# Performance work log

Hardware: AMD Instinct MI355X
Metric: run time of the kernel (lower is better)

The kernel has to match this reference:

```python
import jax, jax.numpy as jnp
import numpy as np

N_NODES, N_EDGES = 50000, 800000
D_H, D_E, HID = 128, 64, 128  # dim_in = D_H + D_E = 192; hidden_dim2 = D_H + HID = 256


def setup_inputs() -> dict:
    key = jax.random.key(0)
    k1, k2, k3, k4, k5 = jax.random.split(key, 5)
    H = jax.random.normal(k1, (N_NODES, D_H), dtype=jnp.float32)
    idx = jax.random.randint(k2, (2, N_EDGES), 0, N_NODES)
    X_e = jax.random.normal(k3, (N_EDGES, D_E), dtype=jnp.float32)
    # kaiming_normal (fan_in mode, relu gain): std = sqrt(2 / fan_in)
    W1 = jax.random.normal(k4, (D_H + D_E, HID), dtype=jnp.float32) * np.sqrt(2.0 / (D_H + D_E)).astype(np.float32)
    W2 = jax.random.normal(k5, (D_H + HID, HID), dtype=jnp.float32) * np.sqrt(2.0 / (D_H + HID)).astype(np.float32)
    return {"H": H, "idx": idx, "X_e": X_e, "W1": W1, "W2": W2}


def reference(H, idx, X_e, W1, W2):
    # gather source-node embeddings and concat with edge features: [E, d_h + d_e]
    x = jnp.concatenate([H[idx[0]], X_e], axis=1)
    y = jax.nn.relu(x @ W1)                                   # [E, HID]
    # scatter_max into destination nodes; empty segments -> 0 (torch_scatter zero fill).
    y = jax.ops.segment_max(y, idx[1], num_segments=H.shape[0])
    y = jnp.maximum(y, 0.0)  # relu output >= 0, so this only fixes -inf empties
    y = jnp.concatenate([H, y], axis=1)                       # [N, d_h + HID]
    y = jax.nn.relu(y @ W2)                                   # [N, HID]
    return y + H  # residual connection (HID == d_h)
```

## Files before the change

kernel.cpp:

```cpp
#include <hip/hip_runtime.h>
#include <hip/hip_bf16.h>
#include <stdint.h>

#define N_NODES 50000
#define N_EDGES 800000
#define D_H 128
#define D_E 64
#define HID 128

#define MTILE 96
#define SMAX 16
#define N_ETILES ((N_EDGES + MTILE - 1) / MTILE)

#define SCAN_B 512
#define N_CHUNKS ((N_NODES + SCAN_B - 1) / SCAN_B)

typedef __attribute__((ext_vector_type(8))) short bf16x8;
typedef __attribute__((ext_vector_type(4))) short s16x4;
typedef __attribute__((ext_vector_type(4))) float f32x4;
typedef __attribute__((ext_vector_type(4))) int i32x4;

__device__ __forceinline__ unsigned short f2bf(float x) {
    unsigned int u = __float_as_uint(x);
    u += 0x7FFFu + ((u >> 16) & 1u);
    return (unsigned short)(u >> 16);
}

__device__ __forceinline__ bf16x8 pack8(const f32x4 a, const f32x4 b) {
    bf16x8 o = { (short)f2bf(a[0]), (short)f2bf(a[1]), (short)f2bf(a[2]), (short)f2bf(a[3]),
                 (short)f2bf(b[0]), (short)f2bf(b[1]), (short)f2bf(b[2]), (short)f2bf(b[3]) };
    return o;
}

#define NG4 (N_NODES * HID / 4)
#define ND4 (N_NODES / 4)
__global__ void zero_ws(float* __restrict__ gmax, int* __restrict__ deg) {
    const int i = blockIdx.x * blockDim.x + threadIdx.x;
    if (i < NG4) {
        ((f32x4*)gmax)[i] = f32x4{0.f, 0.f, 0.f, 0.f};
    } else if (i < NG4 + ND4) {
        ((i32x4*)deg)[i - NG4] = i32x4{0, 0, 0, 0};
    }
}

#define NHB4 (N_NODES * D_H / 4)
#define NW1 (192 * HID)
#define NW2 (256 * HID)
__global__ void conv_aux(const float* __restrict__ H,
                         const float* __restrict__ W1,
                         const float* __restrict__ W2,
                         unsigned short* __restrict__ Hb,
                         unsigned short* __restrict__ W1t,
                         unsigned short* __restrict__ W2t) {
    const int i = blockIdx.x * blockDim.x + threadIdx.x;
    if (i < NHB4) {
        const f32x4 v = ((const f32x4*)H)[i];
        s16x4 pkv = { (short)f2bf(v[0]), (short)f2bf(v[1]),
                      (short)f2bf(v[2]), (short)f2bf(v[3]) };
        ((s16x4*)Hb)[i] = pkv;
    } else if (i < NHB4 + NW1) {
        const int j = i - NHB4;
        const int n = j / 192, k = j - n * 192;
        W1t[j] = f2bf(W1[k * HID + n]);
    } else if (i < NHB4 + NW1 + NW2) {
        const int j = i - NHB4 - NW1;
        const int n = j >> 8, k = j & 255;
        W2t[j] = f2bf(W2[k * HID + n]);
    }
}

__global__ void hist(const int* __restrict__ idx, int* __restrict__ deg) {
    const int i = blockIdx.x * blockDim.x + threadIdx.x;
    atomicAdd(&deg[idx[N_EDGES + i]], 1);
}

__global__ void scan_a(const int* __restrict__ deg, int* __restrict__ sc,
                       int* __restrict__ totals) {
    __shared__ int s[SCAN_B];
    const int tid = threadIdx.x;
    const int i = blockIdx.x * SCAN_B + tid;
    const int v = (i < N_NODES) ? deg[i] : 0;
    s[tid] = v;
    __syncthreads();
    for (int o = 1; o < SCAN_B; o <<= 1) {
        int t = (tid >= o) ? s[tid - o] : 0;
        __syncthreads();
        s[tid] += t;
        __syncthreads();
    }
    if (i < N_NODES) sc[i] = s[tid] - v;
    if (tid == SCAN_B - 1) totals[blockIdx.x] = s[SCAN_B - 1];
}

__global__ void scan_b(int* __restrict__ totals) {
    __shared__ int s[128];
    const int tid = threadIdx.x;
    const int v = (tid < N_CHUNKS) ? totals[tid] : 0;
    s[tid] = v;
    __syncthreads();
    for (int o = 1; o < 128; o <<= 1) {
        int t = (tid >= o) ? s[tid - o] : 0;
        __syncthreads();
        s[tid] += t;
        __syncthreads();
    }
    if (tid < N_CHUNKS) totals[tid] = s[tid] - v;
}

__global__ void scan_c(const int* __restrict__ sc, const int* __restrict__ totals,
                       int* __restrict__ cursor) {
    const int i = blockIdx.x * SCAN_B + threadIdx.x;
    if (i < N_NODES) cursor[i] = sc[i] + totals[blockIdx.x];
}

__global__ void scatter(const int* __restrict__ idx, int* __restrict__ cursor,
                        unsigned long long* __restrict__ pk8) {
    int i = blockIdx.x * blockDim.x + threadIdx.x;
    const int s = idx[i];
    const int d = idx[N_EDGES + i];
    const int p = atomicAdd(&cursor[d], 1);
    pk8[p] = (unsigned long long)(unsigned)i |
             ((unsigned long long)(unsigned)s << 20) |
             ((unsigned long long)(unsigned)d << 37);
}

__global__ __launch_bounds__(256, 3)
void edge_sorted(const float* __restrict__ H,
                 const unsigned short* __restrict__ Hb,
                 const float* __restrict__ Xe,
                 const float* __restrict__ W1,
                 const unsigned short* __restrict__ W1t,
                 const unsigned long long* __restrict__ pk8,
                 float* __restrict__ gmax, int useAux) {
    __shared__ unsigned short sX[MTILE][200];
    __shared__ float ymax[SMAX + 1][132];
    __shared__ int rowD[MTILE];
    __shared__ int segNode[SMAX];
    __shared__ int sWaveTot[4];
    __shared__ unsigned char rowG[MTILE];

    const int tid  = threadIdx.x;
    const int wave = tid >> 6;
    const int lane = tid & 63;
    const int p0   = blockIdx.x * MTILE;

    const int col = lane & 15;
    const int kr0 = (lane >> 4) * 8;

    if (useAux) {
        #pragma unroll
        for (int it = 0; it < 6; ++it) {
            const int j   = tid + it * 256;
            const int row = j >> 4;
            const int c8  = (j & 15) * 8;
            int pe = p0 + row; if (pe >= N_EDGES) pe = N_EDGES - 1;
            const int src = (int)((pk8[pe] >> 20) & 0x1FFFFull);
            *(bf16x8*)&sX[row][c8] = *(const bf16x8*)(Hb + (size_t)src * D_H + c8);
        }
    } else {
        #pragma unroll
        for (int it = 0; it < 12; ++it) {
            const int j   = tid + it * 256;
            const int row = j >> 5;
            const int c4  = (j & 31) * 4;
            int pe = p0 + row; if (pe >= N_EDGES) pe = N_EDGES - 1;
            const int src = (int)((pk8[pe] >> 20) & 0x1FFFFull);
            const f32x4 v = *(const f32x4*)(H + (size_t)src * D_H + c4);
            s16x4 pkv = { (short)f2bf(v[0]), (short)f2bf(v[1]),
                          (short)f2bf(v[2]), (short)f2bf(v[3]) };
            *(s16x4*)&sX[row][c4] = pkv;
        }
    }
    #pragma unroll
    for (int it = 0; it < 3; ++it) {
        const int j   = tid + it * 256;
        const int row = j >> 3;
        const int c8  = (j & 7) * 8;
        int pe = p0 + row; if (pe >= N_EDGES) pe = N_EDGES - 1;
        const int e = (int)(pk8[pe] & 0xFFFFFull);
        const float* p = Xe + (size_t)e * D_E + c8;
        *(bf16x8*)&sX[row][128 + c8] = pack8(*(const f32x4*)p, *(const f32x4*)(p + 4));
    }

    bf16x8 bfrag[6][2];
    if (useAux) {
        #pragma unroll
        for (int ks = 0; ks < 6; ++ks)
            #pragma unroll
            for (int nf = 0; nf < 2; ++nf) {
                const int n = wave * 32 + nf * 16 + col;
                bfrag[ks][nf] = *(const bf16x8*)&W1t[(size_t)n * 192 + ks * 32 + kr0];
            }
    } else {
        #pragma unroll
        for (int ks = 0; ks < 6; ++ks)
            #pragma unroll
            for (int nf = 0; nf < 2; ++nf) {
                const int n  = wave * 32 + nf * 16 + col;
                const int kb = ks * 32 + kr0;
                bf16x8 b;
                #pragma unroll
                for (int f = 0; f < 8; ++f) b[f] = (short)f2bf(W1[(kb + f) * HID + n]);
                bfrag[ks][nf] = b;
            }
    }

    const int pe0 = p0 + tid;
    const bool inTile = (tid < MTILE);
    const bool valid  = inTile && (pe0 < N_EDGES);
    int d = 0;
    if (inTile) {
        const int pc = valid ? pe0 : (N_EDGES - 1);
        d = (int)(pk8[pc] >> 37);
        rowD[tid] = d;
    }
    int dp = __shfl_up(d, 1);
    if (lane == 0 && inTile && tid > 0) dp = (int)(pk8[pe0 - 1] >> 37);
    const bool flag = valid && (tid == 0 || d != dp);
    const unsigned long long m = __ballot(flag);
    if (lane == 0) sWaveTot[wave] = (int)__popcll(m);

    for (int i2 = tid; i2 < (SMAX + 1) * 132; i2 += 256) ((float*)ymax)[i2] = 0.f;
    __syncthreads();

    int g = 255;
    if (valid) {
        const unsigned long long le =
            (lane == 63) ? ~0ull : ((1ull << (lane + 1)) - 1);
        g = (int)__popcll(m & le) - 1 + ((wave == 1) ? sWaveTot[0] : 0);
    }
    if (inTile) rowG[tid] = (unsigned char)(valid ? g : 255);
    if (flag && g < SMAX) segNode[g] = d;
    __syncthreads();

    f32x4 acc[6][2];
    #pragma unroll
    for (int mm = 0; mm < 6; ++mm) {
        acc[mm][0] = f32x4{0.f, 0.f, 0.f, 0.f};
        acc[mm][1] = f32x4{0.f, 0.f, 0.f, 0.f};
    }
    const int arow = lane & 15;
    __builtin_amdgcn_s_setprio(1);
    #pragma unroll
    for (int ks = 0; ks < 6; ++ks)
        #pragma unroll
        for (int mm = 0; mm < 6; ++mm) {
            bf16x8 a = *(const bf16x8*)&sX[mm * 16 + arow][ks * 32 + kr0];
            acc[mm][0] = __builtin_amdgcn_mfma_f32_16x16x32_bf16(a, bfrag[ks][0], acc[mm][0], 0, 0, 0);
            acc[mm][1] = __builtin_amdgcn_mfma_f32_16x16x32_bf16(a, bfrag[ks][1], acc[mm][1], 0, 0, 0);
        }
    __builtin_amdgcn_s_setprio(0);

    const int rb = (lane >> 4) * 4;
    const int cb = wave * 32 + col;
    #pragma unroll
    for (int mm = 0; mm < 6; ++mm) {
        const int r0 = mm * 16 + rb;
        const int g0 = rowG[r0];
        const int g3 = rowG[r0 + 3];
        if (g0 == g3) {
            const float v0 = fmaxf(fmaxf(acc[mm][0][0], acc[mm][0][1]),
                                   fmaxf(acc[mm][0][2], acc[mm][0][3]));
            const float v1 = fmaxf(fmaxf(acc[mm][1][0], acc[mm][1][1]),
                                   fmaxf(acc[mm][1][2], acc[mm][1][3]));
            if (g0 < SMAX) {
                if (v0 > 0.f) atomicMax((int*)&ymax[g0][cb],      __float_as_int(v0));
                if (v1 > 0.f) atomicMax((int*)&ymax[g0][cb + 16], __float_as_int(v1));
            } else if (g0 < 255) {
                float* base = gmax + (size_t)rowD[r0] * HID;
                if (v0 > 0.f) atomicMax((int*)(base + cb),      __float_as_int(v0));
                if (v1 > 0.f) atomicMax((int*)(base + cb + 16), __float_as_int(v1));
            }
        } else {
            #pragma unroll
            for (int r = 0; r < 4; ++r) {
                const int gg = rowG[r0 + r];
                const float v0 = acc[mm][0][r];
                const float v1 = acc[mm][1][r];
                if (gg < SMAX) {
                    if (v0 > 0.f) atomicMax((int*)&ymax[gg][cb],      __float_as_int(v0));
                    if (v1 > 0.f) atomicMax((int*)&ymax[gg][cb + 16], __float_as_int(v1));
                } else if (gg < 255) {
                    float* base = gmax + (size_t)rowD[r0 + r] * HID;
                    if (v0 > 0.f) atomicMax((int*)(base + cb),      __float_as_int(v0));
                    if (v1 > 0.f) atomicMax((int*)(base + cb + 16), __float_as_int(v1));
                }
            }
        }
    }
    __syncthreads();

    const int nSeg = sWaveTot[0] + sWaveTot[1];
    const int nS = (nSeg < SMAX) ? nSeg : SMAX;
    for (int i2 = tid; i2 < nS * 128; i2 += 256) {
        const int sg = i2 >> 7;
        const int c  = i2 & 127;
        const float v = ymax[sg][c];
        float* dst = gmax + (size_t)segNode[sg] * HID + c;
        if (sg == 0 || sg == nSeg - 1) {
            if (v > 0.f) atomicMax((int*)dst, __float_as_int(v));
        } else {
            *dst = v;
        }
    }
}

__global__ __launch_bounds__(256, 4)
void node_mlp(const float* __restrict__ H,
              const float* __restrict__ gmax,
              const float* __restrict__ W2,
              const unsigned short* __restrict__ W2t,
              float* __restrict__ out, int useAux) {
    __shared__ unsigned short sA[64][264];

    const int tid  = threadIdx.x;
    const int wave = tid >> 6;
    const int lane = tid & 63;
    const int base = blockIdx.x * 64;

    const int col = lane & 15;
    const int kr0 = (lane >> 4) * 8;
    bf16x8 bfrag[8][2];
    if (useAux) {
        #pragma unroll
        for (int ks = 0; ks < 8; ++ks)
            #pragma unroll
            for (int nf = 0; nf < 2; ++nf) {
                const int n = wave * 32 + nf * 16 + col;
                bfrag[ks][nf] = *(const bf16x8*)&W2t[(size_t)n * 256 + ks * 32 + kr0];
            }
    } else {
        #pragma unroll
        for (int ks = 0; ks < 8; ++ks)
            #pragma unroll
            for (int nf = 0; nf < 2; ++nf) {
                const int n  = wave * 32 + nf * 16 + col;
                const int kb = ks * 32 + kr0;
                bf16x8 b;
                #pragma unroll
                for (int f = 0; f < 8; ++f) b[f] = (short)f2bf(W2[(kb + f) * HID + n]);
                bfrag[ks][nf] = b;
            }
    }

    #pragma unroll
    for (int it = 0; it < 8; ++it) {
        const int i   = tid + it * 256;
        const int row = i >> 5;
        const int c4  = (i & 31) * 4;
        int node = base + row;
        if (node >= N_NODES) node = N_NODES - 1;
        const f32x4 v = *(const f32x4*)(H + (size_t)node * D_H + c4);
        s16x4 pkv = { (short)f2bf(v[0]), (short)f2bf(v[1]),
                      (short)f2bf(v[2]), (short)f2bf(v[3]) };
        *(s16x4*)&sA[row][c4] = pkv;
    }
    #pragma unroll
    for (int it = 0; it < 8; ++it) {
        const int i   = tid + it * 256;
        const int row = i >> 5;
        const int c4  = (i & 31) * 4;
        int node = base + row;
        if (node >= N_NODES) node = N_NODES - 1;
        const f32x4 v = *(const f32x4*)(gmax + (size_t)node * HID + c4);
        s16x4 pkv = { (short)f2bf(v[0]), (short)f2bf(v[1]),
                      (short)f2bf(v[2]), (short)f2bf(v[3]) };
        *(s16x4*)&sA[row][128 + c4] = pkv;
    }
    __syncthreads();

    f32x4 acc[4][2];
    #pragma unroll
    for (int mm = 0; mm < 4; ++mm) {
        acc[mm][0] = f32x4{0.f, 0.f, 0.f, 0.f};
        acc[mm][1] = f32x4{0.f, 0.f, 0.f, 0.f};
    }
    const int arow = lane & 15;
    __builtin_amdgcn_s_setprio(1);
    #pragma unroll
    for (int ks = 0; ks < 8; ++ks)
        #pragma unroll
        for (int mm = 0; mm < 4; ++mm) {
            bf16x8 a = *(const bf16x8*)&sA[mm * 16 + arow][ks * 32 + kr0];
            acc[mm][0] = __builtin_amdgcn_mfma_f32_16x16x32_bf16(a, bfrag[ks][0], acc[mm][0], 0, 0, 0);
            acc[mm][1] = __builtin_amdgcn_mfma_f32_16x16x32_bf16(a, bfrag[ks][1], acc[mm][1], 0, 0, 0);
        }
    __builtin_amdgcn_s_setprio(0);

    const int rb = (lane >> 4) * 4;
    #pragma unroll
    for (int mm = 0; mm < 4; ++mm)
        #pragma unroll
        for (int r = 0; r < 4; ++r) {
            const int node = base + mm * 16 + rb + r;
            if (node < N_NODES) {
                const size_t o = (size_t)node * HID + wave * 32 + col;
                out[o]      = fmaxf(acc[mm][0][r], 0.f) + H[o];
                out[o + 16] = fmaxf(acc[mm][1][r], 0.f) + H[o + 16];
            }
        }
}

extern "C" void kernel_launch(void* const* d_in, const int* in_sizes, int n_in,
                              void* d_out, int out_size, void* d_ws, size_t ws_size,
                              hipStream_t stream) {
    const float* H   = (const float*)d_in[0];
    const int*   idx = (const int*)d_in[1];
    const float* Xe  = (const float*)d_in[2];
    const float* W1  = (const float*)d_in[3];
    const float* W2  = (const float*)d_in[4];
    float* out = (float*)d_out;

    char* ws = (char*)d_ws;
    float* gmax   = (float*)(ws);
    int*   deg    = (int*)(ws + 25600000);
    int*   sc     = (int*)(ws + 25800192);
    int*   totals = (int*)(ws + 26000384);
    unsigned long long* pk8 = (unsigned long long*)(ws + 26000896);
    unsigned short* W1t = (unsigned short*)(ws + 32400896);
    unsigned short* W2t = (unsigned short*)(ws + 32450048);
    unsigned short* Hb  = (unsigned short*)(ws + 32515584);
    const int useAux = (ws_size >= (size_t)45315584) ? 1 : 0;

    zero_ws<<<(NG4 + ND4 + 255) / 256, 256, 0, stream>>>(gmax, deg);
    if (useAux)
        conv_aux<<<(NHB4 + NW1 + NW2 + 255) / 256, 256, 0, stream>>>(H, W1, W2, Hb, W1t, W2t);
    hist<<<N_EDGES / 256, 256, 0, stream>>>(idx, deg);
    scan_a<<<N_CHUNKS, SCAN_B, 0, stream>>>(deg, sc, totals);
    scan_b<<<1, 128, 0, stream>>>(totals);
    scan_c<<<N_CHUNKS, SCAN_B, 0, stream>>>(sc, totals, deg);
    scatter<<<N_EDGES / 256, 256, 0, stream>>>(idx, deg, pk8);
    edge_sorted<<<N_ETILES, 256, 0, stream>>>(H, Hb, Xe, W1, W1t, pk8, gmax, useAux);
    node_mlp<<<(N_NODES + 63) / 64, 256, 0, stream>>>(H, gmax, W2, W2t, out, useAux);
}
```

Before: 254.6 us.

## Halve edge tile to 48 rows, raise occupancy, single-wave segment detection

```diff
diff --git a/kernel.cpp b/kernel.cpp
--- a/kernel.cpp
+++ b/kernel.cpp
@@ -8,7 +8,7 @@
 #define D_E 64
 #define HID 128
 
-#define MTILE 96
+#define MTILE 48
 #define SMAX 16
 #define N_ETILES ((N_EDGES + MTILE - 1) / MTILE)
 
@@ -24,6 +24,12 @@
     unsigned int u = __float_as_uint(x);
     u += 0x7FFFu + ((u >> 16) & 1u);
     return (unsigned short)(u >> 16);
+}
+
+__device__ __forceinline__ s16x4 pack4(const f32x4 v) {
+    s16x4 o = { (short)f2bf(v[0]), (short)f2bf(v[1]),
+                (short)f2bf(v[2]), (short)f2bf(v[3]) };
+    return o;
 }
 
 __device__ __forceinline__ bf16x8 pack8(const f32x4 a, const f32x4 b) {
@@ -54,10 +60,7 @@
                          unsigned short* __restrict__ W2t) {
     const int i = blockIdx.x * blockDim.x + threadIdx.x;
     if (i < NHB4) {
-        const f32x4 v = ((const f32x4*)H)[i];
-        s16x4 pkv = { (short)f2bf(v[0]), (short)f2bf(v[1]),
-                      (short)f2bf(v[2]), (short)f2bf(v[3]) };
-        ((s16x4*)Hb)[i] = pkv;
+        ((s16x4*)Hb)[i] = pack4(((const f32x4*)H)[i]);
     } else if (i < NHB4 + NW1) {
         const int j = i - NHB4;
         const int n = j / 192, k = j - n * 192;
@@ -124,7 +127,7 @@
              ((unsigned long long)(unsigned)d << 37);
 }
 
-__global__ __launch_bounds__(256, 3)
+__global__ __launch_bounds__(256, 5)
 void edge_sorted(const float* __restrict__ H,
                  const unsigned short* __restrict__ Hb,
                  const float* __restrict__ Xe,
@@ -133,10 +136,10 @@
                  const unsigned long long* __restrict__ pk8,
                  float* __restrict__ gmax, int useAux) {
     __shared__ unsigned short sX[MTILE][200];
-    __shared__ float ymax[SMAX + 1][132];
+    __shared__ float ymax[SMAX][132];
     __shared__ int rowD[MTILE];
     __shared__ int segNode[SMAX];
-    __shared__ int sWaveTot[4];
+    __shared__ int sNSeg;
     __shared__ unsigned char rowG[MTILE];
 
     const int tid  = threadIdx.x;
@@ -149,7 +152,7 @@
 
     if (useAux) {
         #pragma unroll
-        for (int it = 0; it < 6; ++it) {
+        for (int it = 0; it < 3; ++it) {
             const int j   = tid + it * 256;
             const int row = j >> 4;
             const int c8  = (j & 15) * 8;
@@ -159,27 +162,52 @@
         }
     } else {
         #pragma unroll
-        for (int it = 0; it < 12; ++it) {
+        for (int it = 0; it < 6; ++it) {
             const int j   = tid + it * 256;
             const int row = j >> 5;
             const int c4  = (j & 31) * 4;
             int pe = p0 + row; if (pe >= N_EDGES) pe = N_EDGES - 1;
             const int src = (int)((pk8[pe] >> 20) & 0x1FFFFull);
             const f32x4 v = *(const f32x4*)(H + (size_t)src * D_H + c4);
-            s16x4 pkv = { (short)f2bf(v[0]), (short)f2bf(v[1]),
-                          (short)f2bf(v[2]), (short)f2bf(v[3]) };
-            *(s16x4*)&sX[row][c4] = pkv;
-        }
-    }
-    #pragma unroll
-    for (int it = 0; it < 3; ++it) {
-        const int j   = tid + it * 256;
-        const int row = j >> 3;
-        const int c8  = (j & 7) * 8;
-        int pe = p0 + row; if (pe >= N_EDGES) pe = N_EDGES - 1;
-        const int e = (int)(pk8[pe] & 0xFFFFFull);
-        const float* p = Xe + (size_t)e * D_E + c8;
-        *(bf16x8*)&sX[row][128 + c8] = pack8(*(const f32x4*)p, *(const f32x4*)(p + 4));
+            *(s16x4*)&sX[row][c4] = pack4(v);
+        }
+    }
+    #pragma unroll
+    for (int it = 0; it < 2; ++it) {
+        const int j = tid + it * 256;
+        if (j < 384) {
+            const int row = j >> 3;
+            const int c8  = (j & 7) * 8;
+            int pe = p0 + row; if (pe >= N_EDGES) pe = N_EDGES - 1;
+            const int e = (int)(pk8[pe] & 0xFFFFFull);
+            const float* p = Xe + (size_t)e * D_E + c8;
+            *(bf16x8*)&sX[row][128 + c8] = pack8(*(const f32x4*)p, *(const f32x4*)(p + 4));
+        }
+    }
+
+    for (int i2 = tid; i2 < SMAX * 132; i2 += 256) ((float*)ymax)[i2] = 0.f;
+
+    if (tid < 64) {
+        const bool inT  = (tid < MTILE);
+        const bool valid = inT && (p0 + tid < N_EDGES);
+        int pc = p0 + tid; if (pc >= N_EDGES) pc = N_EDGES - 1;
+        int d = 0;
+        if (inT) {
+            d = (int)(pk8[pc] >> 37);
+            rowD[tid] = d;
+        }
+        int dp = __shfl_up(d, 1);
+        const bool flag = valid && (tid == 0 || d != dp);
+        const unsigned long long m = __ballot(flag);
+        if (tid == 0) sNSeg = (int)__popcll(m);
+        int g = 255;
+        if (valid) {
+            const unsigned long long le =
+                (lane == 63) ? ~0ull : ((1ull << (lane + 1)) - 1);
+            g = (int)__popcll(m & le) - 1;
+        }
+        if (inT) rowG[tid] = (unsigned char)(valid ? g : 255);
+        if (flag && g < SMAX) segNode[g] = d;
     }
 
     bf16x8 bfrag[6][2];
@@ -204,38 +232,11 @@
                 bfrag[ks][nf] = b;
             }
     }
-
-    const int pe0 = p0 + tid;
-    const bool inTile = (tid < MTILE);
-    const bool valid  = inTile && (pe0 < N_EDGES);
-    int d = 0;
-    if (inTile) {
-        const int pc = valid ? pe0 : (N_EDGES - 1);
-        d = (int)(pk8[pc] >> 37);
-        rowD[tid] = d;
-    }
-    int dp = __shfl_up(d, 1);
-    if (lane == 0 && inTile && tid > 0) dp = (int)(pk8[pe0 - 1] >> 37);
-    const bool flag = valid && (tid == 0 || d != dp);
-    const unsigned long long m = __ballot(flag);
-    if (lane == 0) sWaveTot[wave] = (int)__popcll(m);
-
-    for (int i2 = tid; i2 < (SMAX + 1) * 132; i2 += 256) ((float*)ymax)[i2] = 0.f;
     __syncthreads();
 
-    int g = 255;
-    if (valid) {
-        const unsigned long long le =
-            (lane == 63) ? ~0ull : ((1ull << (lane + 1)) - 1);
-        g = (int)__popcll(m & le) - 1 + ((wave == 1) ? sWaveTot[0] : 0);
-    }
-    if (inTile) rowG[tid] = (unsigned char)(valid ? g : 255);
-    if (flag && g < SMAX) segNode[g] = d;
-    __syncthreads();
-
-    f32x4 acc[6][2];
-    #pragma unroll
-    for (int mm = 0; mm < 6; ++mm) {
+    f32x4 acc[3][2];
+    #pragma unroll
+    for (int mm = 0; mm < 3; ++mm) {
         acc[mm][0] = f32x4{0.f, 0.f, 0.f, 0.f};
         acc[mm][1] = f32x4{0.f, 0.f, 0.f, 0.f};
     }
@@ -244,7 +245,7 @@
     #pragma unroll
     for (int ks = 0; ks < 6; ++ks)
         #pragma unroll
-        for (int mm = 0; mm < 6; ++mm) {
+        for (int mm = 0; mm < 3; ++mm) {
             bf16x8 a = *(const bf16x8*)&sX[mm * 16 + arow][ks * 32 + kr0];
             acc[mm][0] = __builtin_amdgcn_mfma_f32_16x16x32_bf16(a, bfrag[ks][0], acc[mm][0], 0, 0, 0);
             acc[mm][1] = __builtin_amdgcn_mfma_f32_16x16x32_bf16(a, bfrag[ks][1], acc[mm][1], 0, 0, 0);
@@ -254,19 +255,19 @@
     const int rb = (lane >> 4) * 4;
     const int cb = wave * 32 + col;
     #pragma unroll
-    for (int mm = 0; mm < 6; ++mm) {
+    for (int mm = 0; mm < 3; ++mm) {
         const int r0 = mm * 16 + rb;
-        const int g0 = rowG[r0];
-        const int g3 = rowG[r0 + 3];
-        if (g0 == g3) {
+        const int q0 = rowG[r0];
+        const int q3 = rowG[r0 + 3];
+        if (q0 == q3) {
             const float v0 = fmaxf(fmaxf(acc[mm][0][0], acc[mm][0][1]),
                                    fmaxf(acc[mm][0][2], acc[mm][0][3]));
             const float v1 = fmaxf(fmaxf(acc[mm][1][0], acc[mm][1][1]),
                                    fmaxf(acc[mm][1][2], acc[mm][1][3]));
-            if (g0 < SMAX) {
-                if (v0 > 0.f) atomicMax((int*)&ymax[g0][cb],      __float_as_int(v0));
-                if (v1 > 0.f) atomicMax((int*)&ymax[g0][cb + 16], __float_as_int(v1));
-            } else if (g0 < 255) {
+            if (q0 < SMAX) {
+                if (v0 > 0.f) atomicMax((int*)&ymax[q0][cb],      __float_as_int(v0));
+                if (v1 > 0.f) atomicMax((int*)&ymax[q0][cb + 16], __float_as_int(v1));
+            } else if (q0 < 255) {
                 float* base = gmax + (size_t)rowD[r0] * HID;
                 if (v0 > 0.f) atomicMax((int*)(base + cb),      __float_as_int(v0));
                 if (v1 > 0.f) atomicMax((int*)(base + cb + 16), __float_as_int(v1));
@@ -274,13 +275,13 @@
         } else {
             #pragma unroll
             for (int r = 0; r < 4; ++r) {
-                const int gg = rowG[r0 + r];
+                const int qq = rowG[r0 + r];
                 const float v0 = acc[mm][0][r];
                 const float v1 = acc[mm][1][r];
-                if (gg < SMAX) {
-                    if (v0 > 0.f) atomicMax((int*)&ymax[gg][cb],      __float_as_int(v0));
-                    if (v1 > 0.f) atomicMax((int*)&ymax[gg][cb + 16], __float_as_int(v1));
-                } else if (gg < 255) {
+                if (qq < SMAX) {
+                    if (v0 > 0.f) atomicMax((int*)&ymax[qq][cb],      __float_as_int(v0));
+                    if (v1 > 0.f) atomicMax((int*)&ymax[qq][cb + 16], __float_as_int(v1));
+                } else if (qq < 255) {
                     float* base = gmax + (size_t)rowD[r0 + r] * HID;
                     if (v0 > 0.f) atomicMax((int*)(base + cb),      __float_as_int(v0));
                     if (v1 > 0.f) atomicMax((int*)(base + cb + 16), __float_as_int(v1));
@@ -290,17 +291,19 @@
     }
     __syncthreads();
 
-    const int nSeg = sWaveTot[0] + sWaveTot[1];
+    const int nSeg = sNSeg;
     const int nS = (nSeg < SMAX) ? nSeg : SMAX;
-    for (int i2 = tid; i2 < nS * 128; i2 += 256) {
-        const int sg = i2 >> 7;
-        const int c  = i2 & 127;
-        const float v = ymax[sg][c];
-        float* dst = gmax + (size_t)segNode[sg] * HID + c;
+    for (int i2 = tid; i2 < nS * 32; i2 += 256) {
+        const int sg = i2 >> 5;
+        const int c4 = (i2 & 31) * 4;
+        float* dst = gmax + (size_t)segNode[sg] * HID + c4;
+        const f32x4 v = *(const f32x4*)&ymax[sg][c4];
         if (sg == 0 || sg == nSeg - 1) {
-            if (v > 0.f) atomicMax((int*)dst, __float_as_int(v));
+            #pragma unroll
+            for (int q = 0; q < 4; ++q)
+                if (v[q] > 0.f) atomicMax((int*)(dst + q), __float_as_int(v[q]));
         } else {
-            *dst = v;
+            *(f32x4*)dst = v;
         }
     }
 }
@@ -350,10 +353,7 @@
         const int c4  = (i & 31) * 4;
         int node = base + row;
         if (node >= N_NODES) node = N_NODES - 1;
-        const f32x4 v = *(const f32x4*)(H + (size_t)node * D_H + c4);
-        s16x4 pkv = { (short)f2bf(v[0]), (short)f2bf(v[1]),
-                      (short)f2bf(v[2]), (short)f2bf(v[3]) };
-        *(s16x4*)&sA[row][c4] = pkv;
+        *(s16x4*)&sA[row][c4] = pack4(*(const f32x4*)(H + (size_t)node * D_H + c4));
     }
     #pragma unroll
     for (int it = 0; it < 8; ++it) {
@@ -362,10 +362,7 @@
         const int c4  = (i & 31) * 4;
         int node = base + row;
         if (node >= N_NODES) node = N_NODES - 1;
-        const f32x4 v = *(const f32x4*)(gmax + (size_t)node * HID + c4);
-        s16x4 pkv = { (short)f2bf(v[0]), (short)f2bf(v[1]),
-                      (short)f2bf(v[2]), (short)f2bf(v[3]) };
-        *(s16x4*)&sA[row][128 + c4] = pkv;
+        *(s16x4*)&sA[row][128 + c4] = pack4(*(const f32x4*)(gmax + (size_t)node * HID + c4));
     }
     __syncthreads();
 
```

New measurement: 273.7 us. 7.5% more time.
